# Optimization experiments

Hardware: AMD Instinct MI355X
Metric: run time of the kernel (lower is better)

Reference implementation:

```python
import jax, jax.numpy as jnp
import numpy as np

N_ITER = 64   # projected-subgradient iterations of the batched DRO QP solver
LR0 = 0.05    # base step size (diminishing 1/sqrt(t))


def project_simplex(v):
    # Euclidean projection onto {z >= 0, sum z = 1} (sort-based, O(n log n))
    n = v.shape[0]
    u = jnp.sort(v)[::-1]
    css = jnp.cumsum(u) - 1.0
    k = jnp.arange(1, n + 1, dtype=v.dtype)
    cond = (u - css / k) > 0          # prefix-true pattern
    idx = jnp.sum(cond.astype(jnp.int32)) - 1
    theta = jnp.take(css, idx) / jnp.take(k, idx)
    return jnp.maximum(v - theta, 0.0)


def _dro_obj(z, c, lam, ep, y_hat, rho):
    # Tractable TV-DRO counterpart (Ben-Tal et al. 2013) with eta and obj_aux
    # eliminated analytically:
    #   obj_i* = max(-lam, u_i - eta),  u_i = (ep_i.z - c)^2
    #   feasibility: eta >= max_i u_i - lam; objective nondecreasing in eta
    #   => eta* = max_i u_i - lam
    s = ep @ z - c                     # (n_obs,)
    u = s * s
    umax = jnp.max(u)
    inner = jnp.mean(jnp.maximum(-lam, u - umax + lam))
    return (umax - lam) + rho * lam + inner - jnp.dot(y_hat, z)


_grad_obj = jax.grad(_dro_obj, argnums=(0, 1, 2))


def _solve_one(y_hat, ep, rho):
    # Projected subgradient descent on (z in simplex, c free, lam >= 0)
    n_y = y_hat.shape[0]
    z0 = jnp.full((n_y,), 1.0 / n_y, y_hat.dtype)
    c0 = jnp.mean(ep @ z0)
    lam0 = jnp.asarray(1.0, y_hat.dtype)

    def step(carry, t):
        z, c, lam = carry
        gz, gc, glam = _grad_obj(z, c, lam, ep, y_hat, rho)
        lr = LR0 / jnp.sqrt(t + 1.0)
        z = project_simplex(z - lr * gz)
        c = c - lr * gc
        lam = jnp.maximum(lam - lr * glam, 0.0)
        return (z, c, lam), None

    (z, _, _), _ = jax.lax.scan(step, (z0, c0, lam0),
                                jnp.arange(N_ITER, dtype=y_hat.dtype))
    return z


def setup_inputs() -> dict:
    key = jax.random.key(0)
    kx, ky, kw, kb = jax.random.split(key, 4)
    n_obs, n_x, n_y = 2048, 128, 64
    X = jax.random.normal(kx, (n_obs, n_x), jnp.float32)
    Y = jax.random.normal(ky, (n_obs, n_y), jnp.float32)
    W = jax.random.normal(kw, (n_y, n_x), jnp.float32) / np.sqrt(n_x).astype(np.float32)
    b = jax.random.normal(kb, (n_y,), jnp.float32) * 0.01
    rho = jnp.array([0.1], jnp.float32)
    return {"X": X, "Y": Y, "rho": rho, "W": W, "b": b}


def reference(X, Y, rho, W, b):
    # prediction layer: per-sample linear predict (vectorized over n_obs)
    Y_hat = X @ W.T + b                        # (n_obs, n_y)
    ep = Y - Y_hat                             # residuals, shared by all solves
    # batched DRO solve: one convex problem per scenario y_hat_t (vmapped)
    Z_star = jax.vmap(lambda yh: _solve_one(yh, ep, rho[0]))(Y_hat)
    Z_star = jax.lax.stop_gradient(Z_star)     # torch code detaches z_t
    return Z_star, Y_hat
```

## Files before the change

### kernel.cpp

```cpp
#include <hip/hip_runtime.h>

#define NOBS 2048
#define NX   128
#define NY   64
#define BS   8
#define NT   1024
#define NWAVE (NT / 64)
#define NITER 64

template <int CTRL>
__device__ __forceinline__ float dpp_f(float x) {
    return __int_as_float(__builtin_amdgcn_update_dpp(
        0, __float_as_int(x), CTRL, 0xf, 0xf, true));
}
__device__ __forceinline__ float wave_sum64(float v) {
    v += dpp_f<0x111>(v);
    v += dpp_f<0x112>(v);
    v += dpp_f<0x114>(v);
    v += dpp_f<0x118>(v);
    v += dpp_f<0x142>(v);
    v += dpp_f<0x143>(v);
    return v;
}
__device__ __forceinline__ float wave_max64_nonneg(float v) {
    v = fmaxf(v, dpp_f<0x111>(v));
    v = fmaxf(v, dpp_f<0x112>(v));
    v = fmaxf(v, dpp_f<0x114>(v));
    v = fmaxf(v, dpp_f<0x118>(v));
    v = fmaxf(v, dpp_f<0x142>(v));
    v = fmaxf(v, dpp_f<0x143>(v));
    return v;
}

__global__ __launch_bounds__(256) void prep_kernel(
    const float* __restrict__ X, const float* __restrict__ Y,
    const float* __restrict__ W, const float* __restrict__ b,
    float* __restrict__ yhat_out, float* __restrict__ ep, float* __restrict__ epsum)
{
    __shared__ float Xs[4][NX];
    const int t = threadIdx.x;
    const int row0 = blockIdx.x * 4;
    for (int f = t; f < 4 * NX; f += 256)
        Xs[f >> 7][f & 127] = X[(row0 + (f >> 7)) * NX + (f & 127)];
    __syncthreads();

    const int k = t & 63;
    const int r = t >> 6;
    const float4* W4 = reinterpret_cast<const float4*>(W + k * NX);
    const float4* X4 = reinterpret_cast<const float4*>(&Xs[r][0]);
    float acc = 0.f;
    #pragma unroll
    for (int x = 0; x < NX / 4; ++x) {
        float4 wv = W4[x];
        float4 xv = X4[x];
        acc += wv.x * xv.x + wv.y * xv.y + wv.z * xv.z + wv.w * xv.w;
    }
    const float yh = acc + b[k];
    const int i = row0 + r;
    yhat_out[i * NY + k] = yh;
    const float e = Y[i * NY + k] - yh;
    ep[i * NY + k] = e;

    float se = wave_sum64(e);
    if ((t & 63) == 63) atomicAdd(epsum, se);
}

__global__ __launch_bounds__(NT, 4) void solve_kernel(
    const float* __restrict__ ep, const float* __restrict__ yhat,
    const float* __restrict__ epsum, const float* __restrict__ rho_p,
    float* __restrict__ zout)
{
    __shared__ float Zs[BS][NY];
    __shared__ float Yh[BS][NY];
    __shared__ float V[NOBS][BS];
    __shared__ float Rpart[NWAVE][NY][BS];
    __shared__ float redM[NWAVE][BS];
    __shared__ float red2[NWAVE][4 * BS];
    __shared__ float cS[BS], lamS[BS];

    const int t = threadIdx.x;
    const int lane = t & 63;
    const int wv = t >> 6;
    const int sc0 = blockIdx.x * BS;
    const float rho = rho_p[0];

    if (t < BS * NY) {
        const int j = t >> 6, k = t & 63;
        Yh[j][k] = yhat[(sc0 + j) * NY + k];
        Zs[j][k] = 1.0f / 64.0f;
    }
    if (t < BS) {
        cS[t] = epsum[0] * (1.0f / 131072.0f);
        lamS[t] = 1.0f;
    }
    __syncthreads();

    const int i0 = t;
    const int i1 = t + NT;
    const float4* ep4 = reinterpret_cast<const float4*>(ep);

    for (int it = 0; it < NITER; ++it) {
        const float lr = 0.05f / sqrtf((float)it + 1.0f);

        float s0[BS], s1[BS];
        #pragma unroll
        for (int j = 0; j < BS; ++j) { s0[j] = 0.f; s1[j] = 0.f; }
        #pragma unroll 4
        for (int k4 = 0; k4 < NY / 4; ++k4) {
            const float4 ea = ep4[i0 * (NY / 4) + k4];
            const float4 eb = ep4[i1 * (NY / 4) + k4];
            #pragma unroll
            for (int j = 0; j < BS; ++j) {
                const float4 zv = *reinterpret_cast<const float4*>(&Zs[j][k4 * 4]);
                s0[j] += ea.x * zv.x + ea.y * zv.y + ea.z * zv.z + ea.w * zv.w;
                s1[j] += eb.x * zv.x + eb.y * zv.y + eb.z * zv.z + eb.w * zv.w;
            }
        }
        float lamR[BS];
        #pragma unroll
        for (int j = 0; j < BS; ++j) {
            const float cj = cS[j];
            lamR[j] = lamS[j];
            s0[j] -= cj; s1[j] -= cj;
        }

        #pragma unroll
        for (int j = 0; j < BS; ++j) {
            float pm = fmaxf(s0[j] * s0[j], s1[j] * s1[j]);
            pm = wave_max64_nonneg(pm);
            if (lane == 63) redM[wv][j] = pm;
        }
        __syncthreads();

        float mv = 0.f;
        if (lane < BS) {
            #pragma unroll
            for (int w = 0; w < NWAVE; ++w) mv = fmaxf(mv, redM[w][lane]);
        }
        float umaxR[BS];
        #pragma unroll
        for (int j = 0; j < BS; ++j) umaxR[j] = __shfl(mv, j, 64);

        #pragma unroll
        for (int j = 0; j < BS; ++j) {
            const float um = umaxR[j], lm = lamR[j];
            float pa = 0.f, pe = 0.f, pas = 0.f, pes = 0.f;
            {
                const float s = s0[j], u = s * s;
                const float x = (u - um) + lm;
                const float a = (x > -lm) ? 1.0f : ((x == -lm) ? 0.5f : 0.0f);
                const float e = (u == um) ? 1.0f : 0.0f;
                pa += a; pe += e; pas += a * s; pes += e * s;
            }
            {
                const float s = s1[j], u = s * s;
                const float x = (u - um) + lm;
                const float a = (x > -lm) ? 1.0f : ((x == -lm) ? 0.5f : 0.0f);
                const float e = (u == um) ? 1.0f : 0.0f;
                pa += a; pe += e; pas += a * s; pes += e * s;
            }
            pa = wave_sum64(pa); pe = wave_sum64(pe);
            pas = wave_sum64(pas); pes = wave_sum64(pes);
            if (lane == 63) {
                red2[wv][j]          = pa;  red2[wv][BS + j]     = pe;
                red2[wv][2 * BS + j] = pas; red2[wv][3 * BS + j] = pes;
            }
        }
        __syncthreads();

        float sv = 0.f;
        if (lane < 4 * BS) {
            #pragma unroll
            for (int w = 0; w < NWAVE; ++w) sv += red2[w][lane];
        }
        float wAr[BS], gcKeep = 0.f, glamKeep = 0.f;
        #pragma unroll
        for (int j = 0; j < BS; ++j) {
            const float sumA   = __shfl(sv, j, 64);
            const float sumEq  = __shfl(sv, BS + j, 64);
            const float sumAS  = __shfl(sv, 2 * BS + j, 64);
            const float sumEqS = __shfl(sv, 3 * BS + j, 64);
            const float abar = sumA * (1.0f / (float)NOBS);
            const float wA = (1.0f - abar) / sumEq;
            wAr[j] = wA;
            if (lane == j) {
                gcKeep   = -2.0f * (sumAS * (1.0f / (float)NOBS) + wA * sumEqS);
                glamKeep = (rho - 2.0f) + 2.0f * abar;
            }
        }
        if (wv == 0 && lane < BS) {
            cS[lane]  = cS[lane] - lr * gcKeep;
            lamS[lane] = fmaxf(lamS[lane] - lr * glamKeep, 0.0f);
        }

        {
            float v0[BS], v1[BS];
            #pragma unroll
            for (int j = 0; j < BS; ++j) {
                const float um = umaxR[j], lm = lamR[j], wA = wAr[j];
                {
                    const float s = s0[j], u = s * s;
                    const float x = (u - um) + lm;
                    const float a = (x > -lm) ? 1.0f : ((x == -lm) ? 0.5f : 0.0f);
                    const float e = (u == um) ? 1.0f : 0.0f;
                    v0[j] = (a * (1.0f / (float)NOBS) + e * wA) * s;
                }
                {
                    const float s = s1[j], u = s * s;
                    const float x = (u - um) + lm;
                    const float a = (x > -lm) ? 1.0f : ((x == -lm) ? 0.5f : 0.0f);
                    const float e = (u == um) ? 1.0f : 0.0f;
                    v1[j] = (a * (1.0f / (float)NOBS) + e * wA) * s;
                }
            }
            *reinterpret_cast<float4*>(&V[i0][0]) = make_float4(v0[0], v0[1], v0[2], v0[3]);
            *reinterpret_cast<float4*>(&V[i0][4]) = make_float4(v0[4], v0[5], v0[6], v0[7]);
            *reinterpret_cast<float4*>(&V[i1][0]) = make_float4(v1[0], v1[1], v1[2], v1[3]);
            *reinterpret_cast<float4*>(&V[i1][4]) = make_float4(v1[4], v1[5], v1[6], v1[7]);
        }
        __syncthreads();

        {
            float rp[BS];
            #pragma unroll
            for (int j = 0; j < BS; ++j) rp[j] = 0.f;
            const int ibeg = wv * (NOBS / NWAVE);
            #pragma unroll 4
            for (int ii = 0; ii < NOBS / NWAVE; ++ii) {
                const int i = ibeg + ii;
                const float e = ep[i * NY + lane];
                const float4 va = *reinterpret_cast<const float4*>(&V[i][0]);
                const float4 vb = *reinterpret_cast<const float4*>(&V[i][4]);
                rp[0] += e * va.x; rp[1] += e * va.y; rp[2] += e * va.z; rp[3] += e * va.w;
                rp[4] += e * vb.x; rp[5] += e * vb.y; rp[6] += e * vb.z; rp[7] += e * vb.w;
            }
            *reinterpret_cast<float4*>(&Rpart[wv][lane][0]) = make_float4(rp[0], rp[1], rp[2], rp[3]);
            *reinterpret_cast<float4*>(&Rpart[wv][lane][4]) = make_float4(rp[4], rp[5], rp[6], rp[7]);
        }
        __syncthreads();

        if (wv < BS) {
            const int j = wv, k = lane;
            float r = 0.f;
            #pragma unroll
            for (int w = 0; w < NWAVE; ++w) r += Rpart[w][k][j];
            const float gz = 2.0f * r - Yh[j][k];
            const float vz = Zs[j][k] - lr * gz;

            float sv2 = vz;
            #pragma unroll
            for (int sz = 2; sz <= 64; sz <<= 1) {
                #pragma unroll
                for (int st = sz >> 1; st > 0; st >>= 1) {
                    const float other = __shfl_xor(sv2, st, 64);
                    const bool desc = ((lane & sz) == 0);
                    const bool lower = ((lane & st) == 0);
                    const float mx = fmaxf(sv2, other), mn = fminf(sv2, other);
                    sv2 = (lower == desc) ? mx : mn;
                }
            }
            float css = sv2;
            #pragma unroll
            for (int off = 1; off < 64; off <<= 1) {
                const float nb = __shfl_up(css, off, 64);
                if (lane >= off) css += nb;
            }
            css -= 1.0f;
            const bool cond = (sv2 - css / (float)(lane + 1)) > 0.0f;
            const unsigned long long bal = __ballot(cond);
            const int idx = __popcll(bal) - 1;
            const float cssIdx = __shfl(css, idx, 64);
            const float theta = cssIdx / (float)(idx + 1);
            Zs[j][k] = fmaxf(vz - theta, 0.0f);
        }
        __syncthreads();
    }

    if (t < BS * NY) {
        const int j = t >> 6, k = t & 63;
        zout[(sc0 + j) * NY + k] = Zs[j][k];
    }
}

extern "C" void kernel_launch(void* const* d_in, const int* in_sizes, int n_in,
                              void* d_out, int out_size, void* d_ws, size_t ws_size,
                              hipStream_t stream) {
    const float* X   = (const float*)d_in[0];
    const float* Y   = (const float*)d_in[1];
    const float* rho = (const float*)d_in[2];
    const float* W   = (const float*)d_in[3];
    const float* b   = (const float*)d_in[4];

    float* out   = (float*)d_out;
    float* zout  = out;
    float* yhat  = out + NOBS * NY;
    float* ep    = (float*)d_ws;
    float* epsum = ep + NOBS * NY;

    hipMemsetAsync(epsum, 0, sizeof(float), stream);
    prep_kernel<<<NOBS / 4, 256, 0, stream>>>(X, Y, W, b, yhat, ep, epsum);
    solve_kernel<<<NOBS / BS, NT, 0, stream>>>(ep, yhat, epsum, rho, zout);
}
```

Before: 2.231 ms.

## Compute ep^T V reduction with split-bf16 MFMA instead of scalar FMAs

The per-iteration gradient reduction r = ep^T V over 2048 observations now runs on MFMA 16x16x32 bf16 instructions. Each fp32 operand is split into bf16 hi and lo parts, and three MFMAs per tile approximate fp32 accuracy. The prep kernel writes ep in a pre-swizzled hi/lo bf16 layout matched to the MFMA A-operand, and V is stored transposed in LDS as bf16 pairs. This replaces the FMA-bound scalar loop and the 16-way partial-sum buffer with a 4-way one, at the cost of some precision loss from dropping the lo*lo term.

```diff
diff --git a/kernel.cpp b/kernel.cpp
--- a/kernel.cpp
+++ b/kernel.cpp
@@ -7,6 +7,17 @@
 #define NT   1024
 #define NWAVE (NT / 64)
 #define NITER 64
+
+typedef short short8 __attribute__((ext_vector_type(8)));
+typedef float f32x4 __attribute__((ext_vector_type(4)));
+
+__device__ __forceinline__ unsigned short bf16_rne(float x) {
+    unsigned u = __float_as_uint(x);
+    return (unsigned short)((u + 0x7FFFu + ((u >> 16) & 1u)) >> 16);
+}
+__device__ __forceinline__ float bf16_tof(unsigned short h) {
+    return __uint_as_float(((unsigned)h) << 16);
+}
 
 template <int CTRL>
 __device__ __forceinline__ float dpp_f(float x) {
@@ -35,7 +46,8 @@
 __global__ __launch_bounds__(256) void prep_kernel(
     const float* __restrict__ X, const float* __restrict__ Y,
     const float* __restrict__ W, const float* __restrict__ b,
-    float* __restrict__ yhat_out, float* __restrict__ ep, float* __restrict__ epsum)
+    float* __restrict__ yhat_out, float* __restrict__ ep, float* __restrict__ epsum,
+    unsigned short* __restrict__ epT_hi, unsigned short* __restrict__ epT_lo)
 {
     __shared__ float Xs[4][NX];
     const int t = threadIdx.x;
@@ -61,6 +73,18 @@
     const float e = Y[i * NY + k] - yh;
     ep[i * NY + k] = e;
 
+    {
+        const unsigned short hi = bf16_rne(e);
+        const unsigned short lo = bf16_rne(e - bf16_tof(hi));
+        const int m  = k >> 4;
+        const int q  = i >> 5;
+        const int lc = (k & 15) + 16 * ((i >> 3) & 3);
+        const int d  = i & 7;
+        const int idx = ((m * 64 + q) * 64 + lc) * 8 + d;
+        epT_hi[idx] = hi;
+        epT_lo[idx] = lo;
+    }
+
     float se = wave_sum64(e);
     if ((t & 63) == 63) atomicAdd(epsum, se);
 }
@@ -68,15 +92,18 @@
 __global__ __launch_bounds__(NT, 4) void solve_kernel(
     const float* __restrict__ ep, const float* __restrict__ yhat,
     const float* __restrict__ epsum, const float* __restrict__ rho_p,
+    const unsigned short* __restrict__ epT_hi, const unsigned short* __restrict__ epT_lo,
     float* __restrict__ zout)
 {
     __shared__ float Zs[BS][NY];
     __shared__ float Yh[BS][NY];
-    __shared__ float V[NOBS][BS];
-    __shared__ float Rpart[NWAVE][NY][BS];
+    __shared__ unsigned short VT_hi[BS][2056];
+    __shared__ unsigned short VT_lo[BS][2056];
+    __shared__ float Rp2[4][4][64][4];
     __shared__ float redM[NWAVE][BS];
     __shared__ float red2[NWAVE][4 * BS];
     __shared__ float cS[BS], lamS[BS];
+    __shared__ __align__(16) unsigned short zb[8];
 
     const int t = threadIdx.x;
     const int lane = t & 63;
@@ -93,6 +120,7 @@
         cS[t] = epsum[0] * (1.0f / 131072.0f);
         lamS[t] = 1.0f;
     }
+    if (t < 8) zb[t] = 0;
     __syncthreads();
 
     const int i0 = t;
@@ -193,57 +221,63 @@
             lamS[lane] = fmaxf(lamS[lane] - lr * glamKeep, 0.0f);
         }
 
+        #pragma unroll
+        for (int j = 0; j < BS; ++j) {
+            const float um = umaxR[j], lm = lamR[j], wA = wAr[j];
+            float v0j, v1j;
+            {
+                const float s = s0[j], u = s * s;
+                const float x = (u - um) + lm;
+                const float a = (x > -lm) ? 1.0f : ((x == -lm) ? 0.5f : 0.0f);
+                const float e = (u == um) ? 1.0f : 0.0f;
+                v0j = (a * (1.0f / (float)NOBS) + e * wA) * s;
+            }
+            {
+                const float s = s1[j], u = s * s;
+                const float x = (u - um) + lm;
+                const float a = (x > -lm) ? 1.0f : ((x == -lm) ? 0.5f : 0.0f);
+                const float e = (u == um) ? 1.0f : 0.0f;
+                v1j = (a * (1.0f / (float)NOBS) + e * wA) * s;
+            }
+            const unsigned short h0 = bf16_rne(v0j);
+            VT_hi[j][i0] = h0;
+            VT_lo[j][i0] = bf16_rne(v0j - bf16_tof(h0));
+            const unsigned short h1 = bf16_rne(v1j);
+            VT_hi[j][i1] = h1;
+            VT_lo[j][i1] = bf16_rne(v1j - bf16_tof(h1));
+        }
+        __syncthreads();
+
         {
-            float v0[BS], v1[BS];
-            #pragma unroll
-            for (int j = 0; j < BS; ++j) {
-                const float um = umaxR[j], lm = lamR[j], wA = wAr[j];
-                {
-                    const float s = s0[j], u = s * s;
-                    const float x = (u - um) + lm;
-                    const float a = (x > -lm) ? 1.0f : ((x == -lm) ? 0.5f : 0.0f);
-                    const float e = (u == um) ? 1.0f : 0.0f;
-                    v0[j] = (a * (1.0f / (float)NOBS) + e * wA) * s;
-                }
-                {
-                    const float s = s1[j], u = s * s;
-                    const float x = (u - um) + lm;
-                    const float a = (x > -lm) ? 1.0f : ((x == -lm) ? 0.5f : 0.0f);
-                    const float e = (u == um) ? 1.0f : 0.0f;
-                    v1[j] = (a * (1.0f / (float)NOBS) + e * wA) * s;
-                }
-            }
-            *reinterpret_cast<float4*>(&V[i0][0]) = make_float4(v0[0], v0[1], v0[2], v0[3]);
-            *reinterpret_cast<float4*>(&V[i0][4]) = make_float4(v0[4], v0[5], v0[6], v0[7]);
-            *reinterpret_cast<float4*>(&V[i1][0]) = make_float4(v1[0], v1[1], v1[2], v1[3]);
-            *reinterpret_cast<float4*>(&V[i1][4]) = make_float4(v1[4], v1[5], v1[6], v1[7]);
-        }
-        __syncthreads();
-
-        {
-            float rp[BS];
-            #pragma unroll
-            for (int j = 0; j < BS; ++j) rp[j] = 0.f;
-            const int ibeg = wv * (NOBS / NWAVE);
+            const int m = wv & 3;
+            const int g = wv >> 2;
+            const int jb = lane & 15;
+            const int h  = lane >> 4;
+            const bool jvalid = (jb < BS);
+            f32x4 acc = {0.f, 0.f, 0.f, 0.f};
             #pragma unroll 4
-            for (int ii = 0; ii < NOBS / NWAVE; ++ii) {
-                const int i = ibeg + ii;
-                const float e = ep[i * NY + lane];
-                const float4 va = *reinterpret_cast<const float4*>(&V[i][0]);
-                const float4 vb = *reinterpret_cast<const float4*>(&V[i][4]);
-                rp[0] += e * va.x; rp[1] += e * va.y; rp[2] += e * va.z; rp[3] += e * va.w;
-                rp[4] += e * vb.x; rp[5] += e * vb.y; rp[6] += e * vb.z; rp[7] += e * vb.w;
-            }
-            *reinterpret_cast<float4*>(&Rpart[wv][lane][0]) = make_float4(rp[0], rp[1], rp[2], rp[3]);
-            *reinterpret_cast<float4*>(&Rpart[wv][lane][4]) = make_float4(rp[4], rp[5], rp[6], rp[7]);
+            for (int qq = 0; qq < 16; ++qq) {
+                const int q = g * 16 + qq;
+                const int aoff = ((m * 64 + q) * 64 + lane) * 8;
+                const short8 ah = *(const short8*)(epT_hi + aoff);
+                const short8 al = *(const short8*)(epT_lo + aoff);
+                const unsigned short* vh = jvalid ? &VT_hi[jb][(q << 5) + (h << 3)] : zb;
+                const unsigned short* vl = jvalid ? &VT_lo[jb][(q << 5) + (h << 3)] : zb;
+                const short8 bh = *(const short8*)vh;
+                const short8 bl = *(const short8*)vl;
+                acc = __builtin_amdgcn_mfma_f32_16x16x32_bf16(al, bh, acc, 0, 0, 0);
+                acc = __builtin_amdgcn_mfma_f32_16x16x32_bf16(ah, bl, acc, 0, 0, 0);
+                acc = __builtin_amdgcn_mfma_f32_16x16x32_bf16(ah, bh, acc, 0, 0, 0);
+            }
+            *(f32x4*)(&Rp2[g][m][lane][0]) = acc;
         }
         __syncthreads();
 
         if (wv < BS) {
             const int j = wv, k = lane;
-            float r = 0.f;
-            #pragma unroll
-            for (int w = 0; w < NWAVE; ++w) r += Rpart[w][k][j];
+            const int m = k >> 4, p = k & 3, ll = ((k >> 2) & 3) * 16 + j;
+            const float r = Rp2[0][m][ll][p] + Rp2[1][m][ll][p]
+                          + Rp2[2][m][ll][p] + Rp2[3][m][ll][p];
             const float gz = 2.0f * r - Yh[j][k];
             const float vz = Zs[j][k] - lr * gz;
 
@@ -294,10 +328,13 @@
     float* out   = (float*)d_out;
     float* zout  = out;
     float* yhat  = out + NOBS * NY;
-    float* ep    = (float*)d_ws;
+
+    unsigned short* epT_hi = (unsigned short*)d_ws;
+    unsigned short* epT_lo = epT_hi + NY * NOBS;
+    float* ep    = (float*)(epT_lo + NY * NOBS);
     float* epsum = ep + NOBS * NY;
 
     hipMemsetAsync(epsum, 0, sizeof(float), stream);
-    prep_kernel<<<NOBS / 4, 256, 0, stream>>>(X, Y, W, b, yhat, ep, epsum);
-    solve_kernel<<<NOBS / BS, NT, 0, stream>>>(ep, yhat, epsum, rho, zout);
-}
+    prep_kernel<<<NOBS / 4, 256, 0, stream>>>(X, Y, W, b, yhat, ep, epsum, epT_hi, epT_lo);
+    solve_kernel<<<NOBS / BS, NT, 0, stream>>>(ep, yhat, epsum, rho, epT_hi, epT_lo, zout);
+}
```

Measured after the change: 1.892 ms. 1.18x faster.
